# Performance work log

Measured on AMD Instinct MI355X. Metric: run time of the kernel, lower is better.

Reference implementation:

```python
import jax, jax.numpy as jnp
import numpy as np

D_MODEL = 512
N_HEADS = 8
N_KV_HEADS = 2
HEAD_DIM = 64
PITCH_VOCAB = 128


def setup_inputs() -> dict:
    key = jax.random.key(0)
    ks = jax.random.split(key, 6)
    B, T, P = 2, 256, 12
    s = lambda fan_in: 1.0 / np.sqrt(fan_in)
    hidden_states = jax.random.normal(ks[0], (B, T, P, D_MODEL), dtype=jnp.float32)
    Wq = jax.random.normal(ks[1], (D_MODEL, N_HEADS * HEAD_DIM), dtype=jnp.float32) * s(D_MODEL)
    Wk = jax.random.normal(ks[2], (D_MODEL, N_KV_HEADS * HEAD_DIM), dtype=jnp.float32) * s(D_MODEL)
    Wv = jax.random.normal(ks[3], (D_MODEL, N_KV_HEADS * HEAD_DIM), dtype=jnp.float32) * s(D_MODEL)
    Wo = jax.random.normal(ks[4], (N_HEADS * HEAD_DIM, D_MODEL), dtype=jnp.float32) * s(N_HEADS * HEAD_DIM)
    pitch_table = jax.random.normal(ks[5], (PITCH_VOCAB, HEAD_DIM), dtype=jnp.float32)
    return {"hidden_states": hidden_states, "Wq": Wq, "Wk": Wk, "Wv": Wv, "Wo": Wo, "pitch_table": pitch_table}


def reference(hidden_states, Wq, Wk, Wv, Wo, pitch_table):
    B, T, P, C = hidden_states.shape
    H, Hkv, d = N_HEADS, N_KV_HEADS, HEAD_DIM
    rep = H // Hkv

    q = (hidden_states @ Wq).reshape(B, T, P, H, d)
    k = (hidden_states @ Wk).reshape(B, T, P, Hkv, d)
    v = (hidden_states @ Wv).reshape(B, T, P, Hkv, d)

    # GQA repeat_kv: (B,T,P,Hkv,d) -> (B,T,P,H,d)
    k = jnp.repeat(k, rep, axis=3)
    v = jnp.repeat(v, rep, axis=3)

    # additive pitch bias on q and k
    pitch_emb = pitch_table[jnp.arange(P)]  # (P, d)
    bias = pitch_emb[None, None, :, None, :]
    q = q + bias
    k = k + bias

    # flatten (T,P) -> S and move heads forward: (B,H,S,d)
    S = T * P
    q = q.transpose(0, 3, 1, 2, 4).reshape(B, H, S, d)
    k = k.transpose(0, 3, 1, 2, 4).reshape(B, H, S, d)
    v = v.transpose(0, 3, 1, 2, 4).reshape(B, H, S, d)

    scale = 1.0 / jnp.sqrt(jnp.asarray(d, dtype=q.dtype))
    attn = jax.nn.softmax(jnp.einsum('bhqd,bhkd->bhqk', q, k) * scale, axis=-1)
    out = jnp.einsum('bhqk,bhkd->bhqd', attn, v)  # (B,H,S,d)

    out = out.reshape(B, H, T, P, d).transpose(0, 2, 3, 1, 4).reshape(B, T, P, H * d)
    return out @ Wo
```

## Files before the change

### kernel.cpp

```cpp
#include <hip/hip_runtime.h>
#include <hip/hip_fp16.h>

#define B_   2
#define T_   256
#define P_   12
#define C_   512
#define H_   8
#define HKV_ 2
#define D_   64
#define S_   (T_ * P_)
#define M_   (B_ * S_)
#define NQKV 768

typedef _Float16 half8_t __attribute__((ext_vector_type(8)));
typedef _Float16 half4_t __attribute__((ext_vector_type(4)));
typedef _Float16 half2_t __attribute__((ext_vector_type(2)));
typedef float    float4_t __attribute__((ext_vector_type(4)));

#if __has_builtin(__builtin_amdgcn_exp2f)
#define EXP2(x) __builtin_amdgcn_exp2f(x)
#else
#define EXP2(x) __expf((x) * 0.69314718f)
#endif

#define SOFT_SHIFT 20.0f
#define SOFT_CLAMP2 15.5f
#define QSCALE (0.125f * 1.44269504f)

__global__ __launch_bounds__(256) void prep_kernel(
    const float* __restrict__ hs,
    const float* __restrict__ Wq, const float* __restrict__ Wk,
    const float* __restrict__ Wv, const float* __restrict__ Wo,
    _Float16* __restrict__ hs16,
    _Float16* __restrict__ wcatT,
    _Float16* __restrict__ woT)
{
    const int blk = blockIdx.x;
    const int tid = threadIdx.x;

    if (blk < 160) {
        __shared__ __attribute__((aligned(16))) _Float16 Ts[64][72];
        int t, K;
        const float* src; int srcN, col0; _Float16* dst;
        if (blk < 96) { t = blk; K = 512; dst = wcatT;
            int nt = t / 8;
            int kt = t % 8;
            int n0 = nt * 64, k0 = kt * 64;
            if (n0 < 512)      { src = Wq; srcN = 512; col0 = n0; }
            else if (n0 < 640) { src = Wk; srcN = 128; col0 = n0 - 512; }
            else               { src = Wv; srcN = 128; col0 = n0 - 640; }
#pragma unroll
            for (int i = 0; i < 4; ++i) {
                int row = i * 16 + (tid >> 4);
                int cg  = tid & 15;
                float4_t v = *(const float4_t*)(src + (size_t)(k0 + row) * srcN + col0 + cg * 4);
                Ts[cg * 4 + 0][row] = (_Float16)v[0];
                Ts[cg * 4 + 1][row] = (_Float16)v[1];
                Ts[cg * 4 + 2][row] = (_Float16)v[2];
                Ts[cg * 4 + 3][row] = (_Float16)v[3];
            }
            __syncthreads();
#pragma unroll
            for (int i = 0; i < 2; ++i) {
                int seg = i * 256 + tid;
                int row = seg >> 3, s = seg & 7;
                *(half8_t*)(dst + (size_t)(n0 + row) * K + k0 + s * 8) =
                    *(const half8_t*)&Ts[row][s * 8];
            }
        } else { t = blk - 96; K = 512; dst = woT;
            int nt = t / 8, kt = t % 8;
            int n0 = nt * 64, k0 = kt * 64;
#pragma unroll
            for (int i = 0; i < 4; ++i) {
                int row = i * 16 + (tid >> 4);
                int cg  = tid & 15;
                float4_t v = *(const float4_t*)(Wo + (size_t)(k0 + row) * 512 + n0 + cg * 4);
                Ts[cg * 4 + 0][row] = (_Float16)v[0];
                Ts[cg * 4 + 1][row] = (_Float16)v[1];
                Ts[cg * 4 + 2][row] = (_Float16)v[2];
                Ts[cg * 4 + 3][row] = (_Float16)v[3];
            }
            __syncthreads();
#pragma unroll
            for (int i = 0; i < 2; ++i) {
                int seg = i * 256 + tid;
                int row = seg >> 3, s = seg & 7;
                *(half8_t*)(dst + (size_t)(n0 + row) * K + k0 + s * 8) =
                    *(const half8_t*)&Ts[row][s * 8];
            }
        }
    } else {
        int base = (blk - 160) * 4096;
#pragma unroll
        for (int i = 0; i < 16; ++i) {
            int f4 = base + i * 256 + tid;
            float4_t v = *(const float4_t*)(hs + (size_t)f4 * 4);
            half4_t hv;
            hv[0] = (_Float16)v[0]; hv[1] = (_Float16)v[1];
            hv[2] = (_Float16)v[2]; hv[3] = (_Float16)v[3];
            *(half4_t*)(hs16 + (size_t)f4 * 4) = hv;
        }
    }
}

__global__ __launch_bounds__(256) void qkv_kernel(
    const _Float16* __restrict__ A,
    const _Float16* __restrict__ WT,
    const float* __restrict__ pitch,
    _Float16* __restrict__ qb,
    _Float16* __restrict__ kb,
    _Float16* __restrict__ vb)
{
    const int m0   = blockIdx.x * 64;
    const int n0   = blockIdx.y * 64;
    const int tid  = threadIdx.x;
    const int wave = tid >> 6;
    const int lane = tid & 63;
    const int ln   = lane & 15;
    const int quad = lane >> 4;

    __shared__ __attribute__((aligned(16))) _Float16 As[64][72];
    __shared__ __attribute__((aligned(16))) _Float16 Bs[64][72];

    float4_t acc[4];
#pragma unroll
    for (int nt = 0; nt < 4; ++nt) acc[nt] = (float4_t){0.f, 0.f, 0.f, 0.f};

    const int srow = tid >> 3;
    const int ss   = tid & 7;

    half8_t ar[2], br[2];
#pragma unroll
    for (int i = 0; i < 2; ++i) {
        int row = i * 32 + srow;
        ar[i] = *(const half8_t*)&A [(size_t)(m0 + row) * 512 + ss * 8];
        br[i] = *(const half8_t*)&WT[(size_t)(n0 + row) * 512 + ss * 8];
    }

    for (int k0 = 0; k0 < 512; k0 += 64) {
        __syncthreads();
#pragma unroll
        for (int i = 0; i < 2; ++i) {
            int row = i * 32 + srow;
            *(half8_t*)&As[row][ss * 8] = ar[i];
            *(half8_t*)&Bs[row][ss * 8] = br[i];
        }
        __syncthreads();

        if (k0 + 64 < 512) {
#pragma unroll
            for (int i = 0; i < 2; ++i) {
                int row = i * 32 + srow;
                ar[i] = *(const half8_t*)&A [(size_t)(m0 + row) * 512 + k0 + 64 + ss * 8];
                br[i] = *(const half8_t*)&WT[(size_t)(n0 + row) * 512 + k0 + 64 + ss * 8];
            }
        }

#pragma unroll
        for (int ks = 0; ks < 2; ++ks) {
            half8_t afrag = *(const half8_t*)&As[wave * 16 + ln][ks * 32 + quad * 8];
#pragma unroll
            for (int nt = 0; nt < 4; ++nt) {
                half8_t bfrag = *(const half8_t*)&Bs[nt * 16 + ln][ks * 32 + quad * 8];
                acc[nt] = __builtin_amdgcn_mfma_f32_16x16x32_f16(afrag, bfrag, acc[nt], 0, 0, 0);
            }
        }
    }

    const int region = (n0 < 512) ? 0 : (n0 < 640 ? 1 : 2);
#pragma unroll
    for (int nt = 0; nt < 4; ++nt) {
        int n = n0 + nt * 16 + ln;
#pragma unroll
        for (int r = 0; r < 4; ++r) {
            int m = m0 + wave * 16 + quad * 4 + r;
            int b = m / S_;
            int s = m - b * S_;
            int p = s % P_;
            float v = acc[nt][r];
            if (region == 0) {
                int h = n >> 6, dd = n & 63;
                v = (v + pitch[p * 64 + dd]) * QSCALE;
                qb[(((size_t)(b * H_ + h)) * S_ + s) * 64 + dd] = (_Float16)v;
            } else if (region == 1) {
                int nn = n - 512, h = nn >> 6, dd = nn & 63;
                v = v + pitch[p * 64 + dd];
                kb[(((size_t)(b * HKV_ + h)) * S_ + s) * 64 + dd] = (_Float16)v;
            } else {
                int nn = n - 640, h = nn >> 6, dd = nn & 63;
                vb[(((size_t)(b * HKV_ + h)) * 64 + dd) * S_ + s] = (_Float16)v;
            }
        }
    }
}

__global__ __launch_bounds__(512) void attn_kernel(
    const _Float16* __restrict__ qbuf,
    const _Float16* __restrict__ kbuf,
    const _Float16* __restrict__ vtb,
    _Float16* __restrict__ ob)
{
    const int qblk = blockIdx.x;
    const int bh   = blockIdx.y;
    const int b    = bh >> 3;
    const int h    = bh & 7;
    const int hkv  = h >> 2;
    const int tid  = threadIdx.x;
    const int w    = tid >> 6;
    const int lane = tid & 63;
    const int ln   = lane & 15;
    const int quad = lane >> 4;

    const _Float16* Q  = qbuf + ((size_t)(b * H_ + h)) * S_ * 64;
    const _Float16* K  = kbuf + ((size_t)(b * HKV_ + hkv)) * S_ * 64;
    const _Float16* Vt = vtb  + ((size_t)(b * HKV_ + hkv)) * 64 * S_;

    __shared__ __attribute__((aligned(16))) _Float16 Ks[128][80];
    __shared__ __attribute__((aligned(16))) _Float16 VT[64][136];
    __shared__ __attribute__((aligned(16))) _Float16 Ps[8][16][40];

    const int qbase = qblk * 64 + (w & 3) * 16;
    const int kk0   = (w >> 2) * 32;

    half8_t qfrag[2];
#pragma unroll
    for (int ks = 0; ks < 2; ++ks)
        qfrag[ks] = *(const half8_t*)&Q[(size_t)(qbase + ln) * 64 + ks * 32 + quad * 8];

    float4_t o[4];
#pragma unroll
    for (int nt = 0; nt < 4; ++nt) o[nt] = (float4_t){0.f, 0.f, 0.f, 0.f};
    float lr[4] = {0.f, 0.f, 0.f, 0.f};

    const int j = tid >> 3, s = tid & 7;
    const int r0 = ((j & 1) << 4) | ((j >> 5) << 5) | ((j >> 1) & 15);

    half8_t kr0, kr1, vr0, vr1;
    kr0 = *(const half8_t*)&K[(size_t)j * 64 + s * 8];
    kr1 = *(const half8_t*)&K[(size_t)(64 + j) * 64 + s * 8];
    vr0 = *(const half8_t*)&Vt[(size_t)j * S_ + s * 8];
    vr1 = *(const half8_t*)&Vt[(size_t)j * S_ + 64 + s * 8];

    for (int kt = 0; kt < S_; kt += 128) {
        __syncthreads();
        *(half8_t*)&Ks[r0][s * 8]      = kr0;
        *(half8_t*)&Ks[r0 + 64][s * 8] = kr1;
        *(half8_t*)&VT[j][s * 8]       = vr0;
        *(half8_t*)&VT[j][64 + s * 8]  = vr1;
        __syncthreads();

        if (kt + 128 < S_) {
            kr0 = *(const half8_t*)&K[(size_t)(kt + 128 + j) * 64 + s * 8];
            kr1 = *(const half8_t*)&K[(size_t)(kt + 128 + 64 + j) * 64 + s * 8];
            vr0 = *(const half8_t*)&Vt[(size_t)j * S_ + kt + 128 + s * 8];
            vr1 = *(const half8_t*)&Vt[(size_t)j * S_ + kt + 128 + 64 + s * 8];
        }

#pragma unroll
        for (int h2 = 0; h2 < 2; ++h2) {
            const int kb = h2 * 64 + kk0;

            float4_t sf[2];
            __builtin_amdgcn_s_setprio(1);
#pragma unroll
            for (int c = 0; c < 2; ++c) {
                sf[c] = (float4_t){-SOFT_SHIFT, -SOFT_SHIFT, -SOFT_SHIFT, -SOFT_SHIFT};
#pragma unroll
                for (int ks = 0; ks < 2; ++ks) {
                    half8_t kf = *(const half8_t*)&Ks[kb + c * 16 + ln][ks * 32 + quad * 8];
                    sf[c] = __builtin_amdgcn_mfma_f32_16x16x32_f16(qfrag[ks], kf, sf[c], 0, 0, 0);
                }
            }
            __builtin_amdgcn_s_setprio(0);

#pragma unroll
            for (int rr = 0; rr < 4; ++rr) {
                float p0 = EXP2(fminf(sf[0][rr], SOFT_CLAMP2));
                float p1 = EXP2(fminf(sf[1][rr], SOFT_CLAMP2));
                lr[rr] += p0 + p1;
                half2_t w2; w2[0] = (_Float16)p0; w2[1] = (_Float16)p1;
                *(half2_t*)&Ps[w][quad * 4 + rr][2 * ln] = w2;
            }

            half8_t pf = *(const half8_t*)&Ps[w][ln][quad * 8];
            __builtin_amdgcn_s_setprio(1);
#pragma unroll
            for (int nt = 0; nt < 4; ++nt) {
                half8_t vf = *(const half8_t*)&VT[nt * 16 + ln][kb + quad * 8];
                o[nt] = __builtin_amdgcn_mfma_f32_16x16x32_f16(pf, vf, o[nt], 0, 0, 0);
            }
            __builtin_amdgcn_s_setprio(0);
        }
    }

    __syncthreads();
    if (w >= 4) {
        float* od = (float*)&Ks[0][0] + (w - 4) * 1024;
#pragma unroll
        for (int nt = 0; nt < 4; ++nt)
            *(float4_t*)&od[lane * 16 + nt * 4] = o[nt];
        float* ld = (float*)&Ps[0][0][0] + (w - 4) * 256;
#pragma unroll
        for (int rr = 0; rr < 4; ++rr)
            ld[lane * 4 + rr] = lr[rr];
    }
    __syncthreads();
    if (w < 4) {
        const float* os = (const float*)&Ks[0][0] + w * 1024;
        const float* ls = (const float*)&Ps[0][0][0] + w * 256;
#pragma unroll
        for (int rr = 0; rr < 4; ++rr) {
            float l = lr[rr] + ls[lane * 4 + rr];
            l += __shfl_xor(l, 1);
            l += __shfl_xor(l, 2);
            l += __shfl_xor(l, 4);
            l += __shfl_xor(l, 8);
            float inv = 1.0f / l;
            int qg = qbase + quad * 4 + rr;
            size_t base = ((size_t)(b * S_ + qg)) * 512 + h * 64;
#pragma unroll
            for (int nt = 0; nt < 4; ++nt) {
                float vsum = o[nt][rr] + os[lane * 16 + nt * 4 + rr];
                ob[base + nt * 16 + ln] = (_Float16)(vsum * inv);
            }
        }
    }
}

__global__ __launch_bounds__(256) void proj_out_kernel(
    const _Float16* __restrict__ A,
    const _Float16* __restrict__ WT,
    float* __restrict__ outp)
{
    const int m0   = blockIdx.x * 64;
    const int n0   = blockIdx.y * 64;
    const int tid  = threadIdx.x;
    const int wave = tid >> 6;
    const int lane = tid & 63;
    const int ln   = lane & 15;
    const int quad = lane >> 4;

    __shared__ __attribute__((aligned(16))) _Float16 As[64][72];
    __shared__ __attribute__((aligned(16))) _Float16 Bs[64][72];

    float4_t acc[4];
#pragma unroll
    for (int nt = 0; nt < 4; ++nt) acc[nt] = (float4_t){0.f, 0.f, 0.f, 0.f};

    const int srow = tid >> 3;
    const int ss   = tid & 7;

    half8_t ar[2], br[2];
#pragma unroll
    for (int i = 0; i < 2; ++i) {
        int row = i * 32 + srow;
        ar[i] = *(const half8_t*)&A [(size_t)(m0 + row) * 512 + ss * 8];
        br[i] = *(const half8_t*)&WT[(size_t)(n0 + row) * 512 + ss * 8];
    }

    for (int k0 = 0; k0 < 512; k0 += 64) {
        __syncthreads();
#pragma unroll
        for (int i = 0; i < 2; ++i) {
            int row = i * 32 + srow;
            *(half8_t*)&As[row][ss * 8] = ar[i];
            *(half8_t*)&Bs[row][ss * 8] = br[i];
        }
        __syncthreads();

        if (k0 + 64 < 512) {
#pragma unroll
            for (int i = 0; i < 2; ++i) {
                int row = i * 32 + srow;
                ar[i] = *(const half8_t*)&A [(size_t)(m0 + row) * 512 + k0 + 64 + ss * 8];
                br[i] = *(const half8_t*)&WT[(size_t)(n0 + row) * 512 + k0 + 64 + ss * 8];
            }
        }

#pragma unroll
        for (int ks = 0; ks < 2; ++ks) {
            half8_t afrag = *(const half8_t*)&As[wave * 16 + ln][ks * 32 + quad * 8];
#pragma unroll
            for (int nt = 0; nt < 4; ++nt) {
                half8_t bfrag = *(const half8_t*)&Bs[nt * 16 + ln][ks * 32 + quad * 8];
                acc[nt] = __builtin_amdgcn_mfma_f32_16x16x32_f16(afrag, bfrag, acc[nt], 0, 0, 0);
            }
        }
    }

#pragma unroll
    for (int nt = 0; nt < 4; ++nt) {
        int n = n0 + nt * 16 + ln;
#pragma unroll
        for (int r = 0; r < 4; ++r) {
            int m = m0 + wave * 16 + quad * 4 + r;
            outp[(size_t)m * 512 + n] = acc[nt][r];
        }
    }
}

extern "C" void kernel_launch(void* const* d_in, const int* in_sizes, int n_in,
                              void* d_out, int out_size, void* d_ws, size_t ws_size,
                              hipStream_t stream) {
    const float* hs    = (const float*)d_in[0];
    const float* Wq    = (const float*)d_in[1];
    const float* Wk    = (const float*)d_in[2];
    const float* Wv    = (const float*)d_in[3];
    const float* Wo    = (const float*)d_in[4];
    const float* pitch = (const float*)d_in[5];
    float* out = (float*)d_out;

    _Float16* hs16  = (_Float16*)d_ws;
    _Float16* o_buf = hs16;
    _Float16* q_buf = hs16 + (size_t)M_ * 512;
    _Float16* k_buf = q_buf + (size_t)B_ * H_ * S_ * 64;
    _Float16* v_buf = k_buf + (size_t)B_ * HKV_ * S_ * 64;
    _Float16* wcatT = v_buf + (size_t)B_ * HKV_ * S_ * 64;
    _Float16* woT   = wcatT + (size_t)NQKV * 512;

    prep_kernel<<<352, 256, 0, stream>>>(hs, Wq, Wk, Wv, Wo, hs16, wcatT, woT);
    qkv_kernel<<<dim3(M_ / 64, NQKV / 64), 256, 0, stream>>>(hs16, wcatT, pitch, q_buf, k_buf, v_buf);
    attn_kernel<<<dim3(S_ / 64, B_ * H_), 512, 0, stream>>>(q_buf, k_buf, v_buf, o_buf);
    proj_out_kernel<<<dim3(M_ / 64, 8), 256, 0, stream>>>(o_buf, woT, out);
}
```

Measured before the change: 159.3 us.

## Compute transposed QK^T so P stays in registers, drop LDS round-trip

```diff
diff --git a/kernel.cpp b/kernel.cpp
--- a/kernel.cpp
+++ b/kernel.cpp
@@ -215,9 +215,8 @@
     const _Float16* K  = kbuf + ((size_t)(b * HKV_ + hkv)) * S_ * 64;
     const _Float16* Vt = vtb  + ((size_t)(b * HKV_ + hkv)) * 64 * S_;
 
-    __shared__ __attribute__((aligned(16))) _Float16 Ks[128][80];
-    __shared__ __attribute__((aligned(16))) _Float16 VT[64][136];
-    __shared__ __attribute__((aligned(16))) _Float16 Ps[8][16][40];
+    __shared__ __attribute__((aligned(16))) _Float16 Ks[128][72];
+    __shared__ __attribute__((aligned(16))) _Float16 VT[2][64][72];
 
     const int qbase = qblk * 64 + (w & 3) * 16;
     const int kk0   = (w >> 2) * 32;
@@ -230,10 +229,10 @@
     float4_t o[4];
 #pragma unroll
     for (int nt = 0; nt < 4; ++nt) o[nt] = (float4_t){0.f, 0.f, 0.f, 0.f};
-    float lr[4] = {0.f, 0.f, 0.f, 0.f};
+    float lsum = 0.f;
 
     const int j = tid >> 3, s = tid & 7;
-    const int r0 = ((j & 1) << 4) | ((j >> 5) << 5) | ((j >> 1) & 15);
+    const int vbase = 32 * (s >> 2) + 16 * (s & 1) + 4 * ((s >> 1) & 1);
 
     half8_t kr0, kr1, vr0, vr1;
     kr0 = *(const half8_t*)&K[(size_t)j * 64 + s * 8];
@@ -243,10 +242,18 @@
 
     for (int kt = 0; kt < S_; kt += 128) {
         __syncthreads();
-        *(half8_t*)&Ks[r0][s * 8]      = kr0;
-        *(half8_t*)&Ks[r0 + 64][s * 8] = kr1;
-        *(half8_t*)&VT[j][s * 8]       = vr0;
-        *(half8_t*)&VT[j][64 + s * 8]  = vr1;
+        *(half8_t*)&Ks[j][s * 8]      = kr0;
+        *(half8_t*)&Ks[j + 64][s * 8] = kr1;
+        {
+            half4_t lo0 = __builtin_shufflevector(vr0, vr0, 0, 1, 2, 3);
+            half4_t hi0 = __builtin_shufflevector(vr0, vr0, 4, 5, 6, 7);
+            half4_t lo1 = __builtin_shufflevector(vr1, vr1, 0, 1, 2, 3);
+            half4_t hi1 = __builtin_shufflevector(vr1, vr1, 4, 5, 6, 7);
+            *(half4_t*)&VT[0][j][vbase]     = lo0;
+            *(half4_t*)&VT[0][j][vbase + 8] = hi0;
+            *(half4_t*)&VT[1][j][vbase]     = lo1;
+            *(half4_t*)&VT[1][j][vbase + 8] = hi1;
+        }
         __syncthreads();
 
         if (kt + 128 < S_) {
@@ -258,35 +265,39 @@
 
 #pragma unroll
         for (int h2 = 0; h2 < 2; ++h2) {
-            const int kb = h2 * 64 + kk0;
-
-            float4_t sf[2];
+            const int kbase = h2 * 64 + kk0;
+
+            float4_t sf0 = (float4_t){-SOFT_SHIFT, -SOFT_SHIFT, -SOFT_SHIFT, -SOFT_SHIFT};
+            float4_t sf1 = (float4_t){-SOFT_SHIFT, -SOFT_SHIFT, -SOFT_SHIFT, -SOFT_SHIFT};
             __builtin_amdgcn_s_setprio(1);
 #pragma unroll
-            for (int c = 0; c < 2; ++c) {
-                sf[c] = (float4_t){-SOFT_SHIFT, -SOFT_SHIFT, -SOFT_SHIFT, -SOFT_SHIFT};
-#pragma unroll
-                for (int ks = 0; ks < 2; ++ks) {
-                    half8_t kf = *(const half8_t*)&Ks[kb + c * 16 + ln][ks * 32 + quad * 8];
-                    sf[c] = __builtin_amdgcn_mfma_f32_16x16x32_f16(qfrag[ks], kf, sf[c], 0, 0, 0);
-                }
+            for (int ks = 0; ks < 2; ++ks) {
+                half8_t kf0 = *(const half8_t*)&Ks[kbase + ln][ks * 32 + quad * 8];
+                half8_t kf1 = *(const half8_t*)&Ks[kbase + 16 + ln][ks * 32 + quad * 8];
+                sf0 = __builtin_amdgcn_mfma_f32_16x16x32_f16(kf0, qfrag[ks], sf0, 0, 0, 0);
+                sf1 = __builtin_amdgcn_mfma_f32_16x16x32_f16(kf1, qfrag[ks], sf1, 0, 0, 0);
             }
             __builtin_amdgcn_s_setprio(0);
 
-#pragma unroll
-            for (int rr = 0; rr < 4; ++rr) {
-                float p0 = EXP2(fminf(sf[0][rr], SOFT_CLAMP2));
-                float p1 = EXP2(fminf(sf[1][rr], SOFT_CLAMP2));
-                lr[rr] += p0 + p1;
-                half2_t w2; w2[0] = (_Float16)p0; w2[1] = (_Float16)p1;
-                *(half2_t*)&Ps[w][quad * 4 + rr][2 * ln] = w2;
-            }
-
-            half8_t pf = *(const half8_t*)&Ps[w][ln][quad * 8];
+            float e00 = EXP2(fminf(sf0[0], SOFT_CLAMP2));
+            float e01 = EXP2(fminf(sf0[1], SOFT_CLAMP2));
+            float e02 = EXP2(fminf(sf0[2], SOFT_CLAMP2));
+            float e03 = EXP2(fminf(sf0[3], SOFT_CLAMP2));
+            float e10 = EXP2(fminf(sf1[0], SOFT_CLAMP2));
+            float e11 = EXP2(fminf(sf1[1], SOFT_CLAMP2));
+            float e12 = EXP2(fminf(sf1[2], SOFT_CLAMP2));
+            float e13 = EXP2(fminf(sf1[3], SOFT_CLAMP2));
+            lsum += ((e00 + e01) + (e02 + e03)) + ((e10 + e11) + (e12 + e13));
+            half8_t pf;
+            pf[0] = (_Float16)e00; pf[1] = (_Float16)e01;
+            pf[2] = (_Float16)e02; pf[3] = (_Float16)e03;
+            pf[4] = (_Float16)e10; pf[5] = (_Float16)e11;
+            pf[6] = (_Float16)e12; pf[7] = (_Float16)e13;
+
             __builtin_amdgcn_s_setprio(1);
 #pragma unroll
             for (int nt = 0; nt < 4; ++nt) {
-                half8_t vf = *(const half8_t*)&VT[nt * 16 + ln][kb + quad * 8];
+                half8_t vf = *(const half8_t*)&VT[h2][nt * 16 + ln][kk0 + quad * 8];
                 o[nt] = __builtin_amdgcn_mfma_f32_16x16x32_f16(pf, vf, o[nt], 0, 0, 0);
             }
             __builtin_amdgcn_s_setprio(0);
@@ -294,29 +305,25 @@
     }
 
     __syncthreads();
+    lsum += __shfl_xor(lsum, 16);
+    lsum += __shfl_xor(lsum, 32);
+    float* Lb = (float*)&VT[0][0][0];
+    if (quad == 0) Lb[w * 16 + ln] = lsum;
     if (w >= 4) {
         float* od = (float*)&Ks[0][0] + (w - 4) * 1024;
 #pragma unroll
         for (int nt = 0; nt < 4; ++nt)
             *(float4_t*)&od[lane * 16 + nt * 4] = o[nt];
-        float* ld = (float*)&Ps[0][0][0] + (w - 4) * 256;
-#pragma unroll
-        for (int rr = 0; rr < 4; ++rr)
-            ld[lane * 4 + rr] = lr[rr];
     }
     __syncthreads();
     if (w < 4) {
         const float* os = (const float*)&Ks[0][0] + w * 1024;
-        const float* ls = (const float*)&Ps[0][0][0] + w * 256;
 #pragma unroll
         for (int rr = 0; rr < 4; ++rr) {
-            float l = lr[rr] + ls[lane * 4 + rr];
-            l += __shfl_xor(l, 1);
-            l += __shfl_xor(l, 2);
-            l += __shfl_xor(l, 4);
-            l += __shfl_xor(l, 8);
+            int t = quad * 4 + rr;
+            float l = Lb[w * 16 + t] + Lb[(w + 4) * 16 + t];
             float inv = 1.0f / l;
-            int qg = qbase + quad * 4 + rr;
+            int qg = qbase + t;
             size_t base = ((size_t)(b * S_ + qg)) * 512 + h * 64;
 #pragma unroll
             for (int nt = 0; nt < 4; ++nt) {
```

After: 160.0 us. Within noise of the previous version (+0.4%).

## Specialize QKV epilogue per region, stage V transpose via LDS, repad attention LDS

Applied to the files above, without the earlier changes.

```diff
diff --git a/kernel.cpp b/kernel.cpp
--- a/kernel.cpp
+++ b/kernel.cpp
@@ -167,30 +167,53 @@
         }
     }
 
-    const int region = (n0 < 512) ? 0 : (n0 < 640 ? 1 : 2);
-#pragma unroll
-    for (int nt = 0; nt < 4; ++nt) {
-        int n = n0 + nt * 16 + ln;
+    const int bb      = m0 / S_;
+    const int s00     = m0 - bb * S_;
+    const int sl_base = wave * 16 + quad * 4;
+    const int s_base  = s00 + sl_base;
+    const int p_base  = s_base % P_;
+
+    if (n0 < 512) {
+        const int h = n0 >> 6;
 #pragma unroll
         for (int r = 0; r < 4; ++r) {
-            int m = m0 + wave * 16 + quad * 4 + r;
-            int b = m / S_;
-            int s = m - b * S_;
-            int p = s % P_;
-            float v = acc[nt][r];
-            if (region == 0) {
-                int h = n >> 6, dd = n & 63;
-                v = (v + pitch[p * 64 + dd]) * QSCALE;
-                qb[(((size_t)(b * H_ + h)) * S_ + s) * 64 + dd] = (_Float16)v;
-            } else if (region == 1) {
-                int nn = n - 512, h = nn >> 6, dd = nn & 63;
-                v = v + pitch[p * 64 + dd];
-                kb[(((size_t)(b * HKV_ + h)) * S_ + s) * 64 + dd] = (_Float16)v;
-            } else {
-                int nn = n - 640, h = nn >> 6, dd = nn & 63;
-                vb[(((size_t)(b * HKV_ + h)) * 64 + dd) * S_ + s] = (_Float16)v;
-            }
-        }
+            int p = p_base + r; if (p >= P_) p -= P_;
+            const float* pr = pitch + p * 64;
+            size_t rowb = ((size_t)(bb * H_ + h) * S_ + s_base + r) * 64;
+#pragma unroll
+            for (int nt = 0; nt < 4; ++nt) {
+                int dd = nt * 16 + ln;
+                float v = (acc[nt][r] + pr[dd]) * QSCALE;
+                qb[rowb + dd] = (_Float16)v;
+            }
+        }
+    } else if (n0 < 640) {
+        const int h = (n0 - 512) >> 6;
+#pragma unroll
+        for (int r = 0; r < 4; ++r) {
+            int p = p_base + r; if (p >= P_) p -= P_;
+            const float* pr = pitch + p * 64;
+            size_t rowb = ((size_t)(bb * HKV_ + h) * S_ + s_base + r) * 64;
+#pragma unroll
+            for (int nt = 0; nt < 4; ++nt) {
+                int dd = nt * 16 + ln;
+                kb[rowb + dd] = (_Float16)(acc[nt][r] + pr[dd]);
+            }
+        }
+    } else {
+        const int h = (n0 - 640) >> 6;
+        __syncthreads();
+#pragma unroll
+        for (int nt = 0; nt < 4; ++nt)
+#pragma unroll
+            for (int r = 0; r < 4; ++r)
+                As[nt * 16 + ln][sl_base + r] = (_Float16)acc[nt][r];
+        __syncthreads();
+        const int rw = tid >> 2;
+        const int c0 = (tid & 3) * 16;
+        _Float16* dst = vb + ((size_t)(bb * HKV_ + h) * 64 + rw) * S_ + s00 + c0;
+        *(half8_t*)dst       = *(const half8_t*)&As[rw][c0];
+        *(half8_t*)(dst + 8) = *(const half8_t*)&As[rw][c0 + 8];
     }
 }
 
@@ -216,7 +239,7 @@
     const _Float16* Vt = vtb  + ((size_t)(b * HKV_ + hkv)) * 64 * S_;
 
     __shared__ __attribute__((aligned(16))) _Float16 Ks[128][80];
-    __shared__ __attribute__((aligned(16))) _Float16 VT[64][136];
+    __shared__ __attribute__((aligned(16))) _Float16 VT[2][64][80];
     __shared__ __attribute__((aligned(16))) _Float16 Ps[8][16][40];
 
     const int qbase = qblk * 64 + (w & 3) * 16;
@@ -245,8 +268,8 @@
         __syncthreads();
         *(half8_t*)&Ks[r0][s * 8]      = kr0;
         *(half8_t*)&Ks[r0 + 64][s * 8] = kr1;
-        *(half8_t*)&VT[j][s * 8]       = vr0;
-        *(half8_t*)&VT[j][64 + s * 8]  = vr1;
+        *(half8_t*)&VT[0][j][s * 8]    = vr0;
+        *(half8_t*)&VT[1][j][s * 8]    = vr1;
         __syncthreads();
 
         if (kt + 128 < S_) {
@@ -286,7 +309,7 @@
             __builtin_amdgcn_s_setprio(1);
 #pragma unroll
             for (int nt = 0; nt < 4; ++nt) {
-                half8_t vf = *(const half8_t*)&VT[nt * 16 + ln][kb + quad * 8];
+                half8_t vf = *(const half8_t*)&VT[h2][nt * 16 + ln][kk0 + quad * 8];
                 o[nt] = __builtin_amdgcn_mfma_f32_16x16x32_f16(pf, vf, o[nt], 0, 0, 0);
             }
             __builtin_amdgcn_s_setprio(0);
@@ -295,22 +318,25 @@
 
     __syncthreads();
     if (w >= 4) {
-        float* od = (float*)&Ks[0][0] + (w - 4) * 1024;
+        float* od = (float*)&Ks[0][0] + (w - 4) * 1280;
 #pragma unroll
         for (int nt = 0; nt < 4; ++nt)
-            *(float4_t*)&od[lane * 16 + nt * 4] = o[nt];
+            *(float4_t*)&od[lane * 20 + nt * 4] = o[nt];
         float* ld = (float*)&Ps[0][0][0] + (w - 4) * 256;
-#pragma unroll
-        for (int rr = 0; rr < 4; ++rr)
-            ld[lane * 4 + rr] = lr[rr];
+        *(float4_t*)&ld[lane * 4] = (float4_t){lr[0], lr[1], lr[2], lr[3]};
     }
     __syncthreads();
     if (w < 4) {
-        const float* os = (const float*)&Ks[0][0] + w * 1024;
+        const float* os = (const float*)&Ks[0][0] + w * 1280;
         const float* ls = (const float*)&Ps[0][0][0] + w * 256;
+        float4_t ls4 = *(const float4_t*)&ls[lane * 4];
+        float4_t os4[4];
+#pragma unroll
+        for (int nt = 0; nt < 4; ++nt)
+            os4[nt] = *(const float4_t*)&os[lane * 20 + nt * 4];
 #pragma unroll
         for (int rr = 0; rr < 4; ++rr) {
-            float l = lr[rr] + ls[lane * 4 + rr];
+            float l = lr[rr] + ls4[rr];
             l += __shfl_xor(l, 1);
             l += __shfl_xor(l, 2);
             l += __shfl_xor(l, 4);
@@ -320,7 +346,7 @@
             size_t base = ((size_t)(b * S_ + qg)) * 512 + h * 64;
 #pragma unroll
             for (int nt = 0; nt < 4; ++nt) {
-                float vsum = o[nt][rr] + os[lane * 16 + nt * 4 + rr];
+                float vsum = o[nt][rr] + os4[nt][rr];
                 ob[base + nt * 16 + ln] = (_Float16)(vsum * inv);
             }
         }
```

Result: no change. 157.0 us (-1.5%).
